# Kernel optimization log

Measured on AMD Instinct MI355X. Metric: run time of the kernel, lower is better.

## Reference

```python
import jax, jax.numpy as jnp
import numpy as np

B, T, HD, NH, DS = 4, 1024, 1024, 16, 64
DH = HD // NH


def setup_inputs() -> dict:
    key = jax.random.key(0)
    ks = jax.random.split(key, 12)
    inp = {
        "data": jax.random.normal(ks[0], (B, T, HD), dtype=jnp.float32),
        "scratch_in": jax.random.normal(ks[1], (B, NH, T, DS), dtype=jnp.float32),
        "qkv_w": jax.random.normal(ks[2], (3 * HD, HD), dtype=jnp.float32) * 0.02,
        "qkv_b": jnp.zeros((3 * HD,), dtype=jnp.float32),
        "out_w": jax.random.normal(ks[3], (HD, HD), dtype=jnp.float32) * 0.02,
        "out_b": jnp.zeros((HD,), dtype=jnp.float32),
        "Wq_s": jax.random.normal(ks[4], (NH, DS, DS), dtype=jnp.float32) * 0.02,
        "Wk_s": jax.random.normal(ks[5], (NH, DS, DS), dtype=jnp.float32) * 0.02,
        "Wv_s": jax.random.normal(ks[6], (NH, DS, DS), dtype=jnp.float32) * 0.02,
        "lambda_s": jnp.float32(0.5),  # buffer; > 1e-8 so gate active
        "per_head_scratch_val": jnp.zeros((NH,), dtype=jnp.float32),
    }
    return inp


def reference(data, scratch_in, qkv_w, qkv_b, out_w, out_b, Wq_s, Wk_s, Wv_s, lambda_s, per_head_scratch_val):
    b, t, hd = data.shape
    nh = Wq_s.shape[0]
    dh = hd // nh
    ds = Wq_s.shape[1]

    qkv = data @ qkv_w.T + qkv_b  # [b, t, 3*hd]
    q, k, v = jnp.split(qkv, 3, axis=2)
    Qc = q.reshape(b, t, nh, dh).transpose(0, 2, 1, 3)  # [b, nh, t, dh]
    Kc = k.reshape(b, t, nh, dh).transpose(0, 2, 1, 3)
    Vc = v.reshape(b, t, nh, dh).transpose(0, 2, 1, 3)

    Qs = jnp.einsum('bhts,hsd->bhtd', scratch_in, Wq_s)
    Ks = jnp.einsum('bhts,hsd->bhtd', scratch_in, Wk_s)
    Vs = jnp.einsum('bhts,hsd->bhtd', scratch_in, Wv_s)

    logits_c = jnp.einsum('bhqd,bhkd->bhqk', Qc, Kc) / jnp.sqrt(jnp.float32(dh))
    logits_s = jnp.einsum('bhqd,bhkd->bhqk', Qs, Ks) / jnp.sqrt(jnp.float32(ds))

    lambda_gate = (lambda_s > 1e-8).astype(logits_c.dtype)
    per_head_val = jnp.exp(per_head_scratch_val).reshape(1, nh, 1, 1)
    scratch_delta = (lambda_gate * lambda_s) * per_head_val * logits_s
    unmasked_logits = logits_c + scratch_delta

    delta_logits_rms = jnp.sqrt(jnp.mean(scratch_delta ** 2))
    row_std_ratio = jnp.mean(jnp.std(logits_s, axis=-1, ddof=1) / (jnp.std(logits_c, axis=-1, ddof=1) + 1e-6))

    causal = jnp.tril(jnp.ones((t, t), dtype=jnp.bool_))  # [t, t]
    total_logits = jnp.where(causal[None, None, :, :], unmasked_logits, -jnp.inf)
    attention_weights = jax.nn.softmax(total_logits, axis=-1)  # [b, nh, t, t]

    content_out = jnp.einsum('bhqk,bhkd->bhqd', attention_weights, Vc)
    scratch_out_mid = jnp.einsum('bhqk,bhkd->bhqd', attention_weights, Vs)

    attn_out = content_out.transpose(0, 2, 1, 3).reshape(b, t, hd)
    attn_out = attn_out @ out_w.T + out_b
    return attn_out, scratch_out_mid, delta_logits_rms, row_std_ratio
```

## Files before the change

### kernel.cpp

```cpp
#include <hip/hip_runtime.h>
#include <math.h>
#include <stdint.h>

#define B_ 4
#define T_ 1024
#define NH_ 16
#define MSZ (4194304)

typedef float f4 __attribute__((ext_vector_type(4)));
typedef float f32x4 __attribute__((ext_vector_type(4)));
typedef __bf16 bf16x8 __attribute__((ext_vector_type(8)));
typedef __bf16 bf16x4 __attribute__((ext_vector_type(4)));

static __device__ __forceinline__ f32x4 mfma16(bf16x8 a, bf16x8 b, f32x4 c) {
    return __builtin_amdgcn_mfma_f32_16x16x32_bf16(a, b, c, 0, 0, 0);
}

static __device__ __forceinline__ void gld16(const void* g, void* l) {
    auto gp = reinterpret_cast<const uint32_t __attribute__((address_space(1)))*>(
        reinterpret_cast<uintptr_t>(g));
    auto lp = reinterpret_cast<uint32_t __attribute__((address_space(3)))*>(
        reinterpret_cast<uintptr_t>(l));
    __builtin_amdgcn_global_load_lds(gp, lp, 16, 0, 0);
}

__global__ void k_zero(float* acc) {
    if (threadIdx.x < 2) acc[threadIdx.x] = 0.f;
}

__global__ __launch_bounds__(256) void k_split(
        const float* __restrict__ data, __bf16* __restrict__ dH, __bf16* __restrict__ dL,
        const float* __restrict__ w1,   __bf16* __restrict__ w1H, __bf16* __restrict__ w1L,
        const float* __restrict__ w2,   __bf16* __restrict__ w2H, __bf16* __restrict__ w2L)
{
    const int gsz = gridDim.x * blockDim.x;
    for (size_t i = blockIdx.x * blockDim.x + threadIdx.x; i < 2097152; i += gsz) {
        const float* s; __bf16 *H, *L; size_t off;
        if (i < 1048576)      { s = data; H = dH;  L = dL;  off = i; }
        else if (i < 1835008) { s = w1;   H = w1H; L = w1L; off = i - 1048576; }
        else                  { s = w2;   H = w2H; L = w2L; off = i - 1835008; }
        f4 v = *(const f4*)(s + off*4);
        bf16x4 h, l;
        #pragma unroll
        for (int j = 0; j < 4; ++j) {
            __bf16 hh = (__bf16)v[j];
            h[j] = hh;
            l[j] = (__bf16)(v[j] - (float)hh);
        }
        *(bf16x4*)(H + off*4) = h;
        *(bf16x4*)(L + off*4) = l;
    }
}

template<int MODE>
__global__ __launch_bounds__(256, 2) void k_gemm(
        const __bf16* __restrict__ AH, const __bf16* __restrict__ AL,
        const __bf16* __restrict__ BH, const __bf16* __restrict__ BL,
        const float* __restrict__ bias,
        __bf16* __restrict__ Qb, __bf16* __restrict__ Kb, __bf16* __restrict__ Vtb,
        float* __restrict__ outf)
{
    __shared__ __bf16 sAH[8192];
    __shared__ __bf16 sAL[8192];
    __shared__ __bf16 sBH[8192];
    __shared__ __bf16 sBL[8192];

    const int tid  = threadIdx.x;
    const int lane = tid & 63;
    const int wid  = tid >> 6;
    const int lr   = lane & 15;
    const int lg   = lane >> 4;
    const int wr   = wid >> 1, wc = wid & 1;
    const int m0 = blockIdx.x * 128;
    const int n0 = blockIdx.y * 128;

    f32x4 acc[4][4];
    #pragma unroll
    for (int i = 0; i < 4; ++i)
        #pragma unroll
        for (int j = 0; j < 4; ++j) acc[i][j] = (f32x4){0.f,0.f,0.f,0.f};

    const int rbase = wid * 32;
    const int srow8 = lane >> 3;
    const int schnk = lane & 7;

    for (int k0 = 0; k0 < 1024; k0 += 64) {
        __syncthreads();
        #pragma unroll
        for (int c = 0; c < 4; ++c) {
            int row = rbase + c*8 + srow8;
            size_t sc_ = (size_t)((schnk ^ (row & 7)) << 4);
            size_t dst = (size_t)(rbase + c*8) * 128;
            size_t asrc = (size_t)(n0 + row) * 2048 + (size_t)k0*2 + sc_;
            size_t bsrc = (size_t)(m0 + row) * 2048 + (size_t)k0*2 + sc_;
            gld16((const char*)AH + asrc, (char*)sAH + dst);
            gld16((const char*)AL + asrc, (char*)sAL + dst);
            gld16((const char*)BH + bsrc, (char*)sBH + dst);
            gld16((const char*)BL + bsrc, (char*)sBL + dst);
        }
        __syncthreads();

        #pragma unroll
        for (int kk = 0; kk < 2; ++kk) {
            bf16x8 ah[4], al[4], bh_[4], bl[4];
            #pragma unroll
            for (int rf = 0; rf < 4; ++rf) {
                int row = wr*64 + rf*16 + lr;
                int byte = row*128 + (((kk*4 + lg) ^ (row & 7)) << 4);
                ah[rf] = *(const bf16x8*)((const char*)sAH + byte);
                al[rf] = *(const bf16x8*)((const char*)sAL + byte);
            }
            #pragma unroll
            for (int n = 0; n < 4; ++n) {
                int row = wc*64 + n*16 + lr;
                int byte = row*128 + (((kk*4 + lg) ^ (row & 7)) << 4);
                bh_[n] = *(const bf16x8*)((const char*)sBH + byte);
                bl[n]  = *(const bf16x8*)((const char*)sBL + byte);
            }
            #pragma unroll
            for (int rf = 0; rf < 4; ++rf)
                #pragma unroll
                for (int n = 0; n < 4; ++n) {
                    acc[rf][n] = mfma16(al[rf], bh_[n], acc[rf][n]);
                    acc[rf][n] = mfma16(ah[rf], bl[n],  acc[rf][n]);
                    acc[rf][n] = mfma16(ah[rf], bh_[n], acc[rf][n]);
                }
        }
    }

    #pragma unroll
    for (int n = 0; n < 4; ++n) {
        int col = m0 + wc*64 + n*16 + lr;
        float bb = bias[col];
        #pragma unroll
        for (int rf = 0; rf < 4; ++rf)
            #pragma unroll
            for (int r = 0; r < 4; ++r) {
                float v = acc[rf][n][r] + bb;
                int trow = n0 + wr*64 + rf*16 + lg*4 + r;
                if (MODE == 1) {
                    outf[(size_t)trow*1024 + col] = v;
                } else {
                    int js = col >> 10;
                    int hh = (col >> 6) & 15;
                    int dd = col & 63;
                    int b  = trow >> 10, t = trow & 1023;
                    int bh = b*16 + hh;
                    __bf16 bv = (__bf16)v;
                    if (js == 0)      Qb [((size_t)bh*1024 + t)*64 + dd] = bv;
                    else if (js == 1) Kb [((size_t)bh*1024 + t)*64 + dd] = bv;
                    else              Vtb[((size_t)bh*64 + dd)*1024 + t] = bv;
                }
            }
    }
}

__global__ __launch_bounds__(256) void k_sproj(const float* __restrict__ sin_,
        const float* __restrict__ Wq, const float* __restrict__ Wk, const float* __restrict__ Wv,
        __bf16* __restrict__ Qsb, __bf16* __restrict__ Ksb, __bf16* __restrict__ Vstb)
{
    __shared__ float inT[64*132];
    __shared__ float Wt[64*68];
    const int tid = threadIdx.x;
    const int tx = tid & 15, ty = tid >> 4;
    const int bh = blockIdx.y;
    const int h  = bh & (NH_-1);
    const int t0 = blockIdx.x * 128;
    const size_t base = ((size_t)bh * T_ + t0) * 64;

    #pragma unroll
    for (int l = 0; l < 8; ++l) {
        int fid = l*256 + tid;
        int row = fid >> 4, c4 = fid & 15;
        f4 a = *(const f4*)&sin_[base + (size_t)row*64 + c4*4];
        #pragma unroll
        for (int j = 0; j < 4; ++j) inT[(c4*4+j)*132 + row] = a[j];
    }

    for (int w = 0; w < 3; ++w) {
        const float* Wp = (w == 0) ? Wq : ((w == 1) ? Wk : Wv);
        __syncthreads();
        #pragma unroll
        for (int l = 0; l < 4; ++l) {
            int fid = l*256 + tid;
            int s = fid >> 4, c4 = fid & 15;
            *(f4*)&Wt[s*68 + c4*4] = *(const f4*)&Wp[(size_t)h*4096 + s*64 + c4*4];
        }
        __syncthreads();
        float acc[8][4] = {};
        #pragma unroll 8
        for (int s = 0; s < 64; ++s) {
            f4 w4 = *(const f4*)&Wt[s*68 + tx*4];
            f4 a0 = *(const f4*)&inT[s*132 + ty*8];
            f4 a1 = *(const f4*)&inT[s*132 + ty*8 + 4];
            #pragma unroll
            for (int r = 0; r < 4; ++r)
                #pragma unroll
                for (int j = 0; j < 4; ++j) {
                    acc[r][j]   += a0[r]*w4[j];
                    acc[4+r][j] += a1[r]*w4[j];
                }
        }
        if (w < 2) {
            __bf16* Op = (w == 0) ? Qsb : Ksb;
            #pragma unroll
            for (int r = 0; r < 8; ++r) {
                bf16x4 v;
                #pragma unroll
                for (int j = 0; j < 4; ++j) v[j] = (__bf16)acc[r][j];
                *(bf16x4*)&Op[base + (size_t)(ty*8+r)*64 + tx*4] = v;
            }
        } else {
            #pragma unroll
            for (int r = 0; r < 8; ++r)
                #pragma unroll
                for (int j = 0; j < 4; ++j)
                    Vstb[((size_t)bh*64 + tx*4+j)*1024 + t0 + ty*8 + r] = (__bf16)acc[r][j];
        }
    }
}

__global__ __launch_bounds__(256, 2) void k_attn(
        const __bf16* __restrict__ Qcb, const __bf16* __restrict__ Kcb, const __bf16* __restrict__ Vtb,
        const __bf16* __restrict__ Qsb, const __bf16* __restrict__ Ksb, const __bf16* __restrict__ Vstb,
        const float* __restrict__ lam, const float* __restrict__ phv,
        __bf16* __restrict__ ctxH, __bf16* __restrict__ ctxL,
        float* __restrict__ out2, float* __restrict__ accum)
{
    __shared__ __bf16 sKC[2][4096];
    __shared__ __bf16 sKS[2][4096];
    __shared__ __bf16 sVC[2][4096];
    __shared__ __bf16 sVS[2][4096];
    __shared__ __bf16 sP [4096];

    const int tid  = threadIdx.x;
    const int lane = tid & 63;
    const int wid  = tid >> 6;
    const int lr   = lane & 15;
    const int lg   = lane >> 4;
    const int bh   = blockIdx.x;
    const int qt   = 15 - blockIdx.y;
    const int h    = bh & (NH_-1);
    const int b    = bh >> 4;
    const int q0   = qt * 64;

    const float lv   = lam[0];
    const float coef = (lv > 1e-8f ? lv : 0.f) * __expf(phv[h]);

    const char* kcB = (const char*)Kcb  + (size_t)bh*1024*128;
    const char* ksB = (const char*)Ksb  + (size_t)bh*1024*128;
    const char* vtB = (const char*)Vtb  + (size_t)bh*64*2048;
    const char* vsB = (const char*)Vstb + (size_t)bh*64*2048;

    const int strow0 = wid*16 + (lane>>3);
    const size_t dsto0 = (size_t)wid*2048;

    auto STAGE = [&](int kt, int buf) {
        const bool pvn = (kt <= qt);
        #pragma unroll
        for (int c = 0; c < 2; ++c) {
            int trow = strow0 + c*8;
            int sc_  = (lane&7) ^ (trow&7);
            size_t dsto = dsto0 + c*1024;
            gld16(kcB + ((size_t)(kt*64 + trow))*128 + sc_*16, (char*)sKC[buf] + dsto);
            gld16(ksB + ((size_t)(kt*64 + trow))*128 + sc_*16, (char*)sKS[buf] + dsto);
            if (pvn) {
                gld16(vtB + (size_t)trow*2048 + kt*128 + sc_*16, (char*)sVC[buf] + dsto);
                gld16(vsB + (size_t)trow*2048 + kt*128 + sc_*16, (char*)sVS[buf] + dsto);
            }
        }
    };

    bf16x8 qcf[2], qsf[2];
    {
        int row = q0 + wid*16 + lr;
        size_t qb = ((size_t)bh*1024 + row)*64;
        #pragma unroll
        for (int hf = 0; hf < 2; ++hf) {
            qcf[hf] = *(const bf16x8*)&Qcb[qb + hf*32 + lg*8];
            qsf[hf] = *(const bf16x8*)&Qsb[qb + hf*32 + lg*8];
        }
    }

    f32x4 Oc[4], Os[4];
    #pragma unroll
    for (int n = 0; n < 4; ++n) { Oc[n] = (f32x4){0,0,0,0}; Os[n] = (f32x4){0,0,0,0}; }

    float m4[4], l4[4];
    float sc_s[4] = {}, qq_c[4] = {}, ss_s[4] = {}, qq_s[4] = {};
    #pragma unroll
    for (int i = 0; i < 4; ++i) { m4[i] = -INFINITY; l4[i] = 0.f; }

    STAGE(0, 0);
    __syncthreads();

    int cur = 0;
    for (int kt = 0; kt < 16; ++kt) {
        const bool pv = (kt <= qt);
        if (kt < 15) STAGE(kt + 1, cur ^ 1);

        float L[4][4];
        #pragma unroll
        for (int n = 0; n < 4; ++n) {
            int krow = n*16 + lr;
            int rswz = krow & 7;
            const char* pc = (const char*)sKC[cur] + krow*128;
            const char* ps = (const char*)sKS[cur] + krow*128;
            bf16x8 kc0 = *(const bf16x8*)(pc + (((lg  ) ^ rswz)<<4));
            bf16x8 kc1 = *(const bf16x8*)(pc + (((lg+4) ^ rswz)<<4));
            bf16x8 ks0 = *(const bf16x8*)(ps + (((lg  ) ^ rswz)<<4));
            bf16x8 ks1 = *(const bf16x8*)(ps + (((lg+4) ^ rswz)<<4));
            f32x4 z = {0.f,0.f,0.f,0.f};
            f32x4 sc = mfma16(qcf[1], kc1, mfma16(qcf[0], kc0, z));
            f32x4 ss = mfma16(qsf[1], ks1, mfma16(qsf[0], ks0, z));
            #pragma unroll
            for (int r = 0; r < 4; ++r) {
                sc_s[r] += sc[r];
                qq_c[r] = fmaf(sc[r], sc[r], qq_c[r]);
                ss_s[r] += ss[r];
                qq_s[r] = fmaf(ss[r], ss[r], qq_s[r]);
                L[n][r] = 0.125f * fmaf(coef, ss[r], sc[r]);
            }
        }

        if (pv) {
            if (kt == qt) {
                #pragma unroll
                for (int n = 0; n < 4; ++n) {
                    int kc = n*16 + lr;
                    #pragma unroll
                    for (int r = 0; r < 4; ++r)
                        if (kc > wid*16 + lg*4 + r) L[n][r] = -INFINITY;
                }
            }

            float fr4[4];
            #pragma unroll
            for (int r = 0; r < 4; ++r) {
                float v = fmaxf(fmaxf(L[0][r], L[1][r]), fmaxf(L[2][r], L[3][r]));
                v = fmaxf(v, __shfl_xor(v, 1));
                v = fmaxf(v, __shfl_xor(v, 2));
                v = fmaxf(v, __shfl_xor(v, 4));
                v = fmaxf(v, __shfl_xor(v, 8));
                float mn = fmaxf(m4[r], v);
                float fr = __expf(m4[r] - mn);
                m4[r] = mn; fr4[r] = fr;
                float ps = 0.f;
                #pragma unroll
                for (int n = 0; n < 4; ++n) {
                    float p = __expf(L[n][r] - mn);
                    L[n][r] = p;
                    ps += p;
                }
                l4[r] = l4[r]*fr + ps;
            }
            #pragma unroll
            for (int n = 0; n < 4; ++n)
                #pragma unroll
                for (int r = 0; r < 4; ++r) {
                    Oc[n][r] *= fr4[r];
                    Os[n][r] *= fr4[r];
                }

            #pragma unroll
            for (int n = 0; n < 4; ++n)
                #pragma unroll
                for (int r = 0; r < 4; ++r) {
                    int prow = wid*16 + lg*4 + r;
                    *((__bf16*)((char*)sP + prow*128 + ((((n*16+lr)>>3) ^ (prow&7))<<4) + (((n*16+lr)&7)<<1))) = (__bf16)L[n][r];
                }

            bf16x8 pa[2];
            {
                int prow = wid*16 + lr;
                const char* pp = (const char*)sP + prow*128;
                pa[0] = *(const bf16x8*)(pp + (((lg  ) ^ (prow&7))<<4));
                pa[1] = *(const bf16x8*)(pp + (((lg+4) ^ (prow&7))<<4));
            }
            #pragma unroll
            for (int n = 0; n < 4; ++n) {
                int vrow = n*16 + lr;
                int rswz = vrow & 7;
                const char* pc = (const char*)sVC[cur] + vrow*128;
                const char* ps = (const char*)sVS[cur] + vrow*128;
                bf16x8 vc0 = *(const bf16x8*)(pc + (((lg  ) ^ rswz)<<4));
                bf16x8 vc1 = *(const bf16x8*)(pc + (((lg+4) ^ rswz)<<4));
                bf16x8 vs0 = *(const bf16x8*)(ps + (((lg  ) ^ rswz)<<4));
                bf16x8 vs1 = *(const bf16x8*)(ps + (((lg+4) ^ rswz)<<4));
                Oc[n] = mfma16(pa[1], vc1, mfma16(pa[0], vc0, Oc[n]));
                Os[n] = mfma16(pa[1], vs1, mfma16(pa[0], vs0, Os[n]));
            }
        }

        __syncthreads();
        cur ^= 1;
    }

    float d2p = qq_s[0] + qq_s[1] + qq_s[2] + qq_s[3];

    #pragma unroll
    for (int r = 0; r < 4; ++r) {
        #pragma unroll
        for (int msk = 1; msk <= 8; msk <<= 1) {
            l4[r]   += __shfl_xor(l4[r],   msk);
            sc_s[r] += __shfl_xor(sc_s[r], msk);
            qq_c[r] += __shfl_xor(qq_c[r], msk);
            ss_s[r] += __shfl_xor(ss_s[r], msk);
            qq_s[r] += __shfl_xor(qq_s[r], msk);
        }
    }

    #pragma unroll
    for (int r = 0; r < 4; ++r) {
        float linv = 1.0f / l4[r];
        int row = q0 + wid*16 + lg*4 + r;
        #pragma unroll
        for (int n = 0; n < 4; ++n) {
            int d = n*16 + lr;
            float oc = Oc[n][r] * linv;
            size_t cidx = (((size_t)b*T_ + row)*NH_ + h)*64 + d;
            __bf16 hv = (__bf16)oc;
            ctxH[cidx] = hv;
            ctxL[cidx] = (__bf16)(oc - (float)hv);
            out2[((size_t)bh*T_ + row)*64 + d] = Os[n][r] * linv;
        }
    }

    float rp = 0.f;
    #pragma unroll
    for (int r = 0; r < 4; ++r) {
        float S1c = 0.125f    * sc_s[r];
        float S2c = 0.015625f * qq_c[r];
        float S1s = 0.125f    * ss_s[r];
        float S2s = 0.015625f * qq_s[r];
        float varc = (S2c - S1c*S1c*(1.f/1024.f)) * (1.f/1023.f);
        float vars = (S2s - S1s*S1s*(1.f/1024.f)) * (1.f/1023.f);
        rp += sqrtf(fmaxf(vars, 0.f)) / (sqrtf(fmaxf(varc, 0.f)) + 1e-6f);
    }
    rp *= (1.f/16.f);

    #pragma unroll
    for (int msk = 1; msk <= 32; msk <<= 1) {
        d2p += __shfl_xor(d2p, msk);
        rp  += __shfl_xor(rp,  msk);
    }
    __syncthreads();
    float* sred = (float*)sP;
    if (lane == 0) { sred[wid] = d2p; sred[4+wid] = rp; }
    __syncthreads();
    if (tid == 0) {
        float td2 = (sred[0]+sred[1]+sred[2]+sred[3]) * coef * coef * 0.015625f;
        float tr  =  sred[4]+sred[5]+sred[6]+sred[7];
        atomicAdd(&accum[0], td2);
        atomicAdd(&accum[1], tr);
    }
}

__global__ void k_fin(const float* __restrict__ acc, float* __restrict__ out) {
    if (threadIdx.x == 0) {
        out[0] = sqrtf(acc[0] * (1.f/67108864.f));
        out[1] = acc[1] * (1.f/65536.f);
    }
}

extern "C" void kernel_launch(void* const* d_in, const int* in_sizes, int n_in,
                              void* d_out, int out_size, void* d_ws, size_t ws_size,
                              hipStream_t stream)
{
    const float* data  = (const float*)d_in[0];
    const float* sin_  = (const float*)d_in[1];
    const float* qkv_w = (const float*)d_in[2];
    const float* qkv_b = (const float*)d_in[3];
    const float* out_w = (const float*)d_in[4];
    const float* out_b = (const float*)d_in[5];
    const float* Wq    = (const float*)d_in[6];
    const float* Wk    = (const float*)d_in[7];
    const float* Wv    = (const float*)d_in[8];
    const float* lam   = (const float*)d_in[9];
    const float* phv   = (const float*)d_in[10];
    float* out = (float*)d_out;
    char*  w   = (char*)d_ws;

    const size_t MB = 1024*1024;
    __bf16* Qcb   = (__bf16*)(w);
    __bf16* Kcb   = (__bf16*)(w + 8*MB);
    __bf16* Vtb   = (__bf16*)(w + 16*MB);
    __bf16* Qsb   = (__bf16*)(w + 24*MB);
    __bf16* Ksb   = (__bf16*)(w + 32*MB);
    __bf16* Vstb  = (__bf16*)(w + 40*MB);
    __bf16* dataH = (__bf16*)(w + 48*MB);
    __bf16* dataL = (__bf16*)(w + 56*MB);
    __bf16* wH    = (__bf16*)(w + 64*MB);
    __bf16* wL    = (__bf16*)(w + 70*MB);
    __bf16* owH   = (__bf16*)(w + 76*MB);
    __bf16* owL   = (__bf16*)(w + 78*MB);
    float*  accum = (float*)(w + 80*MB);

    k_zero   <<<1, 64, 0, stream>>>(accum);
    k_split  <<<2048, 256, 0, stream>>>(data, dataH, dataL, qkv_w, wH, wL, out_w, owH, owL);
    k_gemm<0><<<dim3(24, 32), 256, 0, stream>>>(dataH, dataL, wH, wL, qkv_b, Qcb, Kcb, Vtb, nullptr);
    k_sproj  <<<dim3(8, 64), 256, 0, stream>>>(sin_, Wq, Wk, Wv, Qsb, Ksb, Vstb);
    k_attn   <<<dim3(64, 16), 256, 0, stream>>>(Qcb, Kcb, Vtb, Qsb, Ksb, Vstb, lam, phv,
                                                dataH, dataL, out + (size_t)MSZ, accum);
    k_gemm<1><<<dim3(8, 32), 256, 0, stream>>>(dataH, dataL, owH, owL, out_b, nullptr, nullptr, nullptr, out);
    k_fin    <<<1, 64, 0, stream>>>(accum, out + 2*(size_t)MSZ);
}
```

Measured before the change: 329.2 us.

## Pre-tile GEMM operands into MFMA fragment layout and drop LDS staging

The bf16 hi/lo split kernel and the attention context writer now emit operands in a tiled layout where each 16x32 MFMA fragment is contiguous per wavefront. The GEMM then loads fragments straight from global memory into registers, removing the shared-memory staging, swizzle and barriers. The cost is that there is no LDS reuse across waves, so each wave re-reads its fragments from global/L2, and there is no software prefetch of the next k-chunk.

```diff
diff --git a/kernel.cpp b/kernel.cpp
--- a/kernel.cpp
+++ b/kernel.cpp
@@ -33,22 +33,29 @@
         const float* __restrict__ w1,   __bf16* __restrict__ w1H, __bf16* __restrict__ w1L,
         const float* __restrict__ w2,   __bf16* __restrict__ w2H, __bf16* __restrict__ w2L)
 {
-    const int gsz = gridDim.x * blockDim.x;
-    for (size_t i = blockIdx.x * blockDim.x + threadIdx.x; i < 2097152; i += gsz) {
-        const float* s; __bf16 *H, *L; size_t off;
-        if (i < 1048576)      { s = data; H = dH;  L = dL;  off = i; }
-        else if (i < 1835008) { s = w1;   H = w1H; L = w1L; off = i - 1048576; }
-        else                  { s = w2;   H = w2H; L = w2L; off = i - 1835008; }
-        f4 v = *(const f4*)(s + off*4);
-        bf16x4 h, l;
+    const int lane = threadIdx.x & 63;
+    const int lr = lane & 15, lg = lane >> 4;
+    const int wg = (blockIdx.x * 256 + threadIdx.x) >> 6;
+    const int nw = (gridDim.x * 256) >> 6;
+    for (int t = wg; t < 16384; t += nw) {
+        const float* s; __bf16 *H, *L; int tt;
+        if (t < 8192)       { s = data; H = dH;  L = dL;  tt = t; }
+        else if (t < 14336) { s = w1;   H = w1H; L = w1L; tt = t - 8192; }
+        else                { s = w2;   H = w2H; L = w2L; tt = t - 14336; }
+        int r0 = tt >> 5, c0 = tt & 31;
+        const float* src = s + (size_t)(r0*16 + lr)*1024 + c0*32 + lg*8;
+        f4 a = *(const f4*)src;
+        f4 b = *(const f4*)(src + 4);
+        bf16x8 h, l;
         #pragma unroll
         for (int j = 0; j < 4; ++j) {
-            __bf16 hh = (__bf16)v[j];
-            h[j] = hh;
-            l[j] = (__bf16)(v[j] - (float)hh);
-        }
-        *(bf16x4*)(H + off*4) = h;
-        *(bf16x4*)(L + off*4) = l;
+            __bf16 h1 = (__bf16)a[j];
+            h[j] = h1; l[j] = (__bf16)(a[j] - (float)h1);
+            __bf16 h2 = (__bf16)b[j];
+            h[4+j] = h2; l[4+j] = (__bf16)(b[j] - (float)h2);
+        }
+        *(bf16x8*)(H + (size_t)tt*512 + lane*8) = h;
+        *(bf16x8*)(L + (size_t)tt*512 + lane*8) = l;
     }
 }
 
@@ -60,11 +67,6 @@
         __bf16* __restrict__ Qb, __bf16* __restrict__ Kb, __bf16* __restrict__ Vtb,
         float* __restrict__ outf)
 {
-    __shared__ __bf16 sAH[8192];
-    __shared__ __bf16 sAL[8192];
-    __shared__ __bf16 sBH[8192];
-    __shared__ __bf16 sBL[8192];
-
     const int tid  = threadIdx.x;
     const int lane = tid & 63;
     const int wid  = tid >> 6;
@@ -73,6 +75,8 @@
     const int wr   = wid >> 1, wc = wid & 1;
     const int m0 = blockIdx.x * 128;
     const int n0 = blockIdx.y * 128;
+    const int ar0 = (n0 >> 4) + wr*4;
+    const int br0 = (m0 >> 4) + wc*4;
 
     f32x4 acc[4][4];
     #pragma unroll
@@ -80,52 +84,28 @@
         #pragma unroll
         for (int j = 0; j < 4; ++j) acc[i][j] = (f32x4){0.f,0.f,0.f,0.f};
 
-    const int rbase = wid * 32;
-    const int srow8 = lane >> 3;
-    const int schnk = lane & 7;
-
-    for (int k0 = 0; k0 < 1024; k0 += 64) {
-        __syncthreads();
-        #pragma unroll
-        for (int c = 0; c < 4; ++c) {
-            int row = rbase + c*8 + srow8;
-            size_t sc_ = (size_t)((schnk ^ (row & 7)) << 4);
-            size_t dst = (size_t)(rbase + c*8) * 128;
-            size_t asrc = (size_t)(n0 + row) * 2048 + (size_t)k0*2 + sc_;
-            size_t bsrc = (size_t)(m0 + row) * 2048 + (size_t)k0*2 + sc_;
-            gld16((const char*)AH + asrc, (char*)sAH + dst);
-            gld16((const char*)AL + asrc, (char*)sAL + dst);
-            gld16((const char*)BH + bsrc, (char*)sBH + dst);
-            gld16((const char*)BL + bsrc, (char*)sBL + dst);
-        }
-        __syncthreads();
-
-        #pragma unroll
-        for (int kk = 0; kk < 2; ++kk) {
-            bf16x8 ah[4], al[4], bh_[4], bl[4];
-            #pragma unroll
-            for (int rf = 0; rf < 4; ++rf) {
-                int row = wr*64 + rf*16 + lr;
-                int byte = row*128 + (((kk*4 + lg) ^ (row & 7)) << 4);
-                ah[rf] = *(const bf16x8*)((const char*)sAH + byte);
-                al[rf] = *(const bf16x8*)((const char*)sAL + byte);
-            }
+    for (int c0 = 0; c0 < 32; ++c0) {
+        bf16x8 ah[4], al[4], bh_[4], bl[4];
+        #pragma unroll
+        for (int rf = 0; rf < 4; ++rf) {
+            size_t o = (((size_t)(ar0 + rf)*32 + c0) << 9) + lane*8;
+            ah[rf] = *(const bf16x8*)(AH + o);
+            al[rf] = *(const bf16x8*)(AL + o);
+        }
+        #pragma unroll
+        for (int n = 0; n < 4; ++n) {
+            size_t o = (((size_t)(br0 + n)*32 + c0) << 9) + lane*8;
+            bh_[n] = *(const bf16x8*)(BH + o);
+            bl[n]  = *(const bf16x8*)(BL + o);
+        }
+        #pragma unroll
+        for (int rf = 0; rf < 4; ++rf)
             #pragma unroll
             for (int n = 0; n < 4; ++n) {
-                int row = wc*64 + n*16 + lr;
-                int byte = row*128 + (((kk*4 + lg) ^ (row & 7)) << 4);
-                bh_[n] = *(const bf16x8*)((const char*)sBH + byte);
-                bl[n]  = *(const bf16x8*)((const char*)sBL + byte);
-            }
-            #pragma unroll
-            for (int rf = 0; rf < 4; ++rf)
-                #pragma unroll
-                for (int n = 0; n < 4; ++n) {
-                    acc[rf][n] = mfma16(al[rf], bh_[n], acc[rf][n]);
-                    acc[rf][n] = mfma16(ah[rf], bl[n],  acc[rf][n]);
-                    acc[rf][n] = mfma16(ah[rf], bh_[n], acc[rf][n]);
-                }
-        }
+                acc[rf][n] = mfma16(al[rf], bh_[n], acc[rf][n]);
+                acc[rf][n] = mfma16(ah[rf], bl[n],  acc[rf][n]);
+                acc[rf][n] = mfma16(ah[rf], bh_[n], acc[rf][n]);
+            }
     }
 
     #pragma unroll
@@ -410,6 +390,7 @@
         }
     }
 
+    const int rtile = (b << 6) + (qt << 2) + wid;
     #pragma unroll
     for (int r = 0; r < 4; ++r) {
         float linv = 1.0f / l4[r];
@@ -418,10 +399,14 @@
         for (int n = 0; n < 4; ++n) {
             int d = n*16 + lr;
             float oc = Oc[n][r] * linv;
-            size_t cidx = (((size_t)b*T_ + row)*NH_ + h)*64 + d;
+            int col = h*64 + d;
+            int c0   = col >> 5;
+            int lgp  = (col >> 3) & 3;
+            int lanep = lgp*16 + lg*4 + r;
+            size_t off = (((size_t)rtile*32 + c0) << 9) + lanep*8 + (col & 7);
             __bf16 hv = (__bf16)oc;
-            ctxH[cidx] = hv;
-            ctxL[cidx] = (__bf16)(oc - (float)hv);
+            ctxH[off] = hv;
+            ctxL[off] = (__bf16)(oc - (float)hv);
             out2[((size_t)bh*T_ + row)*64 + d] = Os[n][r] * linv;
         }
     }
```

After: 340.6 us. +3.5%, slower.
